# Performance work log

Measured on AMD Instinct MI355X. Metric: run time of the kernel, lower is better.

## Reference

```python
import jax, jax.numpy as jnp
import numpy as np

B, T, D = 4, 4096, 1024

def setup_inputs() -> dict:
    key = jax.random.key(0)
    ks = jax.random.split(key, 7)
    s1 = 1.0 / np.sqrt(D)
    s2 = 1.0 / np.sqrt(2 * D)
    return {
        "x": jax.random.normal(ks[0], (B, T, D), jnp.float32),
        "W1": jax.random.uniform(ks[1], (D, 2 * D), jnp.float32, -s1, s1),      # Linear(D,2D,bias=False)
        "W2": jax.random.uniform(ks[2], (2 * D, 2 * D), jnp.float32, -s2, s2),  # Linear(2D,2D)
        "b2": jax.random.uniform(ks[3], (2 * D,), jnp.float32, -s2, s2),
        "conv_w": jax.random.uniform(ks[4], (D, 1, 3), jnp.float32, -1/np.sqrt(3), 1/np.sqrt(3)),  # depthwise k=3
        "gamma": jnp.ones((D,), jnp.float32),
        "beta": jnp.zeros((D,), jnp.float32),
    }

def _gated_scan(theta, alpha):
    # parallel stable scan: h_t = a_t * h_{t-1} + (1 - a_t) * tanh(theta_t), h_0 = 0
    a = jax.nn.sigmoid(alpha)
    b = (1.0 - a) * jnp.tanh(theta)
    def combine(c1, c2):
        a1, b1 = c1
        a2, b2 = c2
        return a1 * a2, a2 * b1 + b2
    _, h = jax.lax.associative_scan(combine, (a, b), axis=1)
    return h

def reference(x, W1, W2, b2, conv_w, gamma, beta):
    # morphism generator: Linear -> SiLU -> Linear
    mp = jax.nn.silu(x @ W1) @ W2 + b2                      # (B,T,2D)
    theta, alpha = jnp.split(mp, 2, axis=-1)
    semantic = _gated_scan(theta, alpha)                    # (B,T,D)
    # causal depthwise conv: left-pad 2, kernel 3, groups=D
    sc = jnp.transpose(semantic, (0, 2, 1))                 # (B,D,T)
    cb = jax.lax.conv_general_dilated(
        sc, conv_w, window_strides=(1,), padding=[(2, 0)],
        dimension_numbers=("NCH", "OIH", "NCH"), feature_group_count=D)
    cb = jax.nn.silu(jnp.transpose(cb, (0, 2, 1)))          # (B,T,D)
    y = semantic + 0.1 * cb
    # LayerNorm over D
    mu = jnp.mean(y, axis=-1, keepdims=True)
    var = jnp.mean(jnp.square(y - mu), axis=-1, keepdims=True)
    y = (y - mu) * jax.lax.rsqrt(var + 1e-5) * gamma + beta
    # dropout is identity in eval mode; L2 normalize (torch eps=1e-12)
    nrm = jnp.sqrt(jnp.sum(jnp.square(y), axis=-1, keepdims=True))
    return y / jnp.maximum(nrm, 1e-12)
```

## Files before the change

kernel.cpp:

```cpp
#include <hip/hip_runtime.h>
#include <cstdint>
#include <cstddef>

typedef __attribute__((ext_vector_type(8))) short bf16x8;
typedef __attribute__((ext_vector_type(4))) float f32x4;
typedef unsigned short u16;
typedef unsigned int u32;

__device__ __forceinline__ u16 f2bf(float f) {
  u32 u = __float_as_uint(f);
  u32 r = (u + 0x7fffu + ((u >> 16) & 1u)) >> 16;
  return (u16)r;
}
__device__ __forceinline__ float bf2f(u16 h) {
  return __uint_as_float(((u32)h) << 16);
}
__device__ __forceinline__ float fsilu(float v) { return v / (1.f + __expf(-v)); }
__device__ __forceinline__ float fsigmoid(float v) { return 1.f / (1.f + __expf(-v)); }
__device__ __forceinline__ float ftanh(float v) {
  return 1.f - 2.f / (__expf(2.f * v) + 1.f);
}

__device__ __forceinline__ void glds16(const void* g, void* l) {
  __builtin_amdgcn_global_load_lds(
      (const __attribute__((address_space(1))) void*)g,
      (__attribute__((address_space(3))) void*)l, 16, 0, 0);
}

#define FENCE_MEM() asm volatile("" ::: "memory")
#define BAR() __builtin_amdgcn_s_barrier()
#define VMCNT(n) asm volatile("s_waitcnt vmcnt(" #n ")" ::: "memory")
#define LGKMW(n)                                        \
  do {                                                  \
    asm volatile("s_waitcnt lgkmcnt(" #n ")" ::: "memory"); \
    __builtin_amdgcn_sched_barrier(0);                  \
  } while (0)


__global__ __launch_bounds__(256) void cast_bf16_vec(const float* __restrict__ src,
                                                     u16* __restrict__ dst, int n4) {
  int i = blockIdx.x * 256 + threadIdx.x;
  if (i >= n4) return;
  const float4 v = ((const float4*)src)[i];
  ushort4 o;
  o.x = f2bf(v.x); o.y = f2bf(v.y); o.z = f2bf(v.z); o.w = f2bf(v.w);
  ((ushort4*)dst)[i] = o;
}

__global__ void transpose_cast(const float* __restrict__ src, u16* __restrict__ dst,
                               int R, int C) {
  __shared__ float tile[32][33];
  int bx = blockIdx.x * 32;
  int by = blockIdx.y * 32;
  int tx = threadIdx.x, ty = threadIdx.y;
#pragma unroll
  for (int i = 0; i < 4; ++i)
    tile[ty + i * 8][tx] = src[(size_t)(by + ty + i * 8) * C + bx + tx];
  __syncthreads();
#pragma unroll
  for (int i = 0; i < 4; ++i)
    dst[(size_t)(bx + ty + i * 8) * R + by + tx] = f2bf(tile[tx][ty + i * 8]);
}


template <int EPI>
__global__ __launch_bounds__(512, 2) void gemm256(const u16* __restrict__ A,
                                                  const u16* __restrict__ Bt,
                                                  u16* __restrict__ Co,
                                                  const float* __restrict__ bias,
                                                  int M, int N, int K) {
  __shared__ char lds[131072];
  const int tid = threadIdx.x;
  const int lane = tid & 63;
  const int wid = tid >> 6;
  const int wr = wid >> 2;
  const int wc = wid & 3;

  const int gx = gridDim.x;
  const int nwg = gx * gridDim.y;
  const int bid = blockIdx.y * gx + blockIdx.x;
  const int swz = (bid & 7) * (nwg >> 3) + (bid >> 3);
  const long bm = (long)(swz / gx) * 256;
  const long bn = (long)(swz % gx) * 256;

  const int NT = K >> 6;

  const int r0 = tid >> 3, c0p = tid & 7;
  const int r1 = r0 + 64;
  const int gA0 = (r0 & 63) + ((r0 >> 6) << 7);
  const int gA1 = (r1 & 63) + ((r1 >> 6) << 7);
  const int gB0 = (r0 & 31) + ((r0 >> 5) << 6);
  const int gB1 = (r1 & 31) + ((r1 >> 5) << 6);
  const int cA0 = c0p ^ (r0 & 7);
  const size_t srcA0 = (size_t)(bm + gA0) * K + cA0 * 8;
  const size_t srcA1 = (size_t)(bm + gA1) * K + cA0 * 8;
  const size_t srcB0 = (size_t)(bn + gB0) * K + cA0 * 8;
  const size_t srcB1 = (size_t)(bn + gB1) * K + cA0 * 8;
  const int dstA0 = gA0 * 128 + c0p * 16;
  const int dstA1 = gA1 * 128 + c0p * 16;
  const int dstB0 = 32768 + gB0 * 128 + c0p * 16;
  const int dstB1 = 32768 + gB1 * 128 + c0p * 16;
  const size_t halfA = (size_t)64 * K;
  const size_t halfB = (size_t)32 * K;

#define STAGE_P(buf, t, pair)                                                        \
  do {                                                                               \
    if ((pair) == 0) {                                                               \
      glds16(A + srcA0 + (size_t)(t) * 64, lds + (buf) * 65536 + dstA0);             \
      glds16(A + srcA1 + (size_t)(t) * 64, lds + (buf) * 65536 + dstA1);             \
    } else if ((pair) == 1) {                                                        \
      glds16(A + srcA0 + halfA + (size_t)(t) * 64,                                   \
             lds + (buf) * 65536 + dstA0 + 8192);                                    \
      glds16(A + srcA1 + halfA + (size_t)(t) * 64,                                   \
             lds + (buf) * 65536 + dstA1 + 8192);                                    \
    } else if ((pair) == 2) {                                                        \
      glds16(Bt + srcB0 + (size_t)(t) * 64, lds + (buf) * 65536 + dstB0);            \
      glds16(Bt + srcB1 + (size_t)(t) * 64, lds + (buf) * 65536 + dstB1);            \
    } else {                                                                         \
      glds16(Bt + srcB0 + halfB + (size_t)(t) * 64,                                  \
             lds + (buf) * 65536 + dstB0 + 4096);                                    \
      glds16(Bt + srcB1 + halfB + (size_t)(t) * 64,                                  \
             lds + (buf) * 65536 + dstB1 + 4096);                                    \
    }                                                                                \
  } while (0)

  const int l15 = lane & 15, l3 = lane & 7, g4 = lane >> 4;
  const int aoff0 = (wr * 128 + l15) * 128 + ((g4 ^ l3) * 16);
  const int aoff1 = (wr * 128 + l15) * 128 + (((4 + g4) ^ l3) * 16);
  const int boff0 = 32768 + (wc * 64 + l15) * 128 + ((g4 ^ l3) * 16);
  const int boff1 = 32768 + (wc * 64 + l15) * 128 + (((4 + g4) ^ l3) * 16);

  f32x4 acc[8][4] = {};

#define READ_A(dst, q)                                                               \
  do {                                                                               \
    dst[0][0] = *(const bf16x8*)(base + aoff0 + ((q) * 2 + 0) * 2048);               \
    dst[0][1] = *(const bf16x8*)(base + aoff1 + ((q) * 2 + 0) * 2048);               \
    dst[1][0] = *(const bf16x8*)(base + aoff0 + ((q) * 2 + 1) * 2048);               \
    dst[1][1] = *(const bf16x8*)(base + aoff1 + ((q) * 2 + 1) * 2048);               \
  } while (0)

#define MFMA_Q(q, af)                                                                \
  do {                                                                               \
    __builtin_amdgcn_s_setprio(1);                                                   \
    _Pragma("unroll") for (int kh = 0; kh < 2; ++kh)                                 \
        _Pragma("unroll") for (int mm = 0; mm < 2; ++mm)                             \
            _Pragma("unroll") for (int nn = 0; nn < 4; ++nn) {                       \
      acc[(q) * 2 + mm][nn] = __builtin_amdgcn_mfma_f32_16x16x32_bf16(               \
          af[mm][kh], bfr[nn][kh], acc[(q) * 2 + mm][nn], 0, 0, 0);                  \
    }                                                                                \
    __builtin_amdgcn_s_setprio(0);                                                   \
  } while (0)

  STAGE_P(0, 0, 0);
  STAGE_P(0, 0, 1);
  STAGE_P(0, 0, 2);
  STAGE_P(0, 0, 3);
  VMCNT(0);
  FENCE_MEM();
  BAR();
  FENCE_MEM();

  for (int t = 0; t < NT; ++t) {
    const int p = t & 1;
    const char* base = lds + p * 65536;
    const bool s1 = (t + 1) < NT;

    bf16x8 bfr[4][2];
    bf16x8 afx[2][2], afy[2][2];

#pragma unroll
    for (int nn = 0; nn < 4; ++nn) {
      bfr[nn][0] = *(const bf16x8*)(base + boff0 + nn * 2048);
      bfr[nn][1] = *(const bf16x8*)(base + boff1 + nn * 2048);
    }
    READ_A(afx, 0);
    READ_A(afy, 1);
    if (s1) STAGE_P(p ^ 1, t + 1, 0);
    FENCE_MEM();
    LGKMW(4);
    MFMA_Q(0, afx);
    READ_A(afx, 2);
    if (s1) STAGE_P(p ^ 1, t + 1, 1);
    FENCE_MEM();
    LGKMW(4);
    MFMA_Q(1, afy);
    READ_A(afy, 3);
    if (s1) STAGE_P(p ^ 1, t + 1, 2);
    FENCE_MEM();
    LGKMW(4);
    MFMA_Q(2, afx);
    if (s1) STAGE_P(p ^ 1, t + 1, 3);
    FENCE_MEM();
    LGKMW(0);
    MFMA_Q(3, afy);

    VMCNT(0);
    FENCE_MEM();
    BAR();
    FENCE_MEM();
  }

  const int erow = (lane >> 4) * 4;
  const int ecol = lane & 15;
#pragma unroll
  for (int mf = 0; mf < 8; ++mf) {
#pragma unroll
    for (int nf = 0; nf < 4; ++nf) {
      const long col = bn + wc * 64 + nf * 16 + ecol;
      float badd = (EPI == 1) ? bias[col] : 0.f;
#pragma unroll
      for (int j = 0; j < 4; ++j) {
        const long row = bm + wr * 128 + mf * 16 + erow + j;
        float v = acc[mf][nf][j];
        if (EPI == 0) {
          v = fsilu(v);
        } else {
          v += badd;
          v = (col < 1024) ? ftanh(v) : fsigmoid(v);
        }
        Co[row * (long)N + col] = f2bf(v);
      }
    }
  }
#undef STAGE_P
#undef READ_A
#undef MFMA_Q
}


__global__ __launch_bounds__(256) void scan_stage1(const u16* __restrict__ sa,
                                                   float* __restrict__ cA,
                                                   float* __restrict__ cB,
                                                   float* __restrict__ cA63,
                                                   float* __restrict__ cB63) {
  const int tid = blockIdx.x * 256 + threadIdx.x;
  const int d = tid & 1023;
  const int chunk = (tid >> 10) & 63;
  const int b = tid >> 16;
  const size_t base = ((size_t)(b * 4096 + chunk * 64)) * 2048 + d;
  float Ac = 1.f, Bc = 0.f;
#pragma unroll 4
  for (int t = 0; t < 63; ++t) {
    float s = bf2f(sa[base + (size_t)t * 2048]);
    float a = bf2f(sa[base + (size_t)t * 2048 + 1024]);
    Bc = a * Bc + (1.f - a) * s;
    Ac *= a;
  }
  cA63[tid] = Ac;
  cB63[tid] = Bc;
  {
    float s = bf2f(sa[base + (size_t)63 * 2048]);
    float a = bf2f(sa[base + (size_t)63 * 2048 + 1024]);
    Bc = a * Bc + (1.f - a) * s;
    Ac *= a;
  }
  cA[tid] = Ac;
  cB[tid] = Bc;
}

__global__ __launch_bounds__(256) void scan_stage2(const float* __restrict__ cA,
                                                   const float* __restrict__ cB,
                                                   float* __restrict__ hstart) {
  const int tid = blockIdx.x * 256 + threadIdx.x;
  const int d = tid & 1023;
  const int b = tid >> 10;
  float h = 0.f;
  for (int c = 0; c < 64; ++c) {
    const size_t i = ((size_t)(b * 64 + c)) * 1024 + d;
    hstart[i] = h;
    h = cA[i] * h + cB[i];
  }
}

__global__ __launch_bounds__(256) void scan3_fused(
    const u16* __restrict__ sa, const float* __restrict__ hstart,
    const float* __restrict__ cA63, const float* __restrict__ cB63,
    const float* __restrict__ cw, const float* __restrict__ gamma,
    const float* __restrict__ beta, float* __restrict__ out) {
  const int blk = blockIdx.x;
  const int c = blk & 63;
  const int tid = threadIdx.x;
  const int lane = tid & 63, wid = tid >> 6;
  const int d0 = tid * 4;
  const size_t m0 = (size_t)(blk >> 6) * 4096 + (size_t)c * 64;

  __shared__ float red[4][8];

  const float4 gv = *(const float4*)(gamma + d0);
  const float4 bv = *(const float4*)(beta + d0);
  const float g[4] = {gv.x, gv.y, gv.z, gv.w};
  const float be[4] = {bv.x, bv.y, bv.z, bv.w};
  float w0[4], w1[4], w2[4];
#pragma unroll
  for (int j = 0; j < 4; ++j) {
    w0[j] = cw[(d0 + j) * 3];
    w1[j] = cw[(d0 + j) * 3 + 1];
    w2[j] = cw[(d0 + j) * 3 + 2];
  }

  const size_t hidx = (size_t)blk * 1024 + d0;
  const float4 hs = *(const float4*)(hstart + hidx);
  float h1v[4] = {hs.x, hs.y, hs.z, hs.w};
  float h2v[4] = {0.f, 0.f, 0.f, 0.f};
  if (c > 0) {
    const float4 hp = *(const float4*)(hstart + hidx - 1024);
    const float4 a63 = *(const float4*)(cA63 + hidx - 1024);
    const float4 b63 = *(const float4*)(cB63 + hidx - 1024);
    h2v[0] = a63.x * hp.x + b63.x;
    h2v[1] = a63.y * hp.y + b63.y;
    h2v[2] = a63.z * hp.z + b63.z;
    h2v[3] = a63.w * hp.w + b63.w;
  }

  float sg2 = 0.f, sgb = 0.f, sb2 = 0.f;
#pragma unroll
  for (int j = 0; j < 4; ++j) {
    sg2 += g[j] * g[j];
    sgb += g[j] * be[j];
    sb2 += be[j] * be[j];
  }
#pragma unroll
  for (int o = 32; o > 0; o >>= 1) {
    sg2 += __shfl_down(sg2, o);
    sgb += __shfl_down(sgb, o);
    sb2 += __shfl_down(sb2, o);
  }
  if (lane == 0) { red[wid][5] = sg2; red[wid][6] = sgb; red[wid][7] = sb2; }
  __syncthreads();
  const float Sg2 = red[0][5] + red[1][5] + red[2][5] + red[3][5];
  const float Sgb = red[0][6] + red[1][6] + red[2][6] + red[3][6];
  const float Sb2 = red[0][7] + red[1][7] + red[2][7] + red[3][7];
  __syncthreads();

  const u16* ps = sa + m0 * 2048 + d0;
  ushort4 sv = *(const ushort4*)(ps);
  ushort4 av = *(const ushort4*)(ps + 1024);

  for (int t = 0; t < 64; ++t) {
    ushort4 svn, avn;
    if (t + 1 < 64) {
      svn = *(const ushort4*)(ps + (size_t)(t + 1) * 2048);
      avn = *(const ushort4*)(ps + (size_t)(t + 1) * 2048 + 1024);
    }
    const float sarr[4] = {bf2f(sv.x), bf2f(sv.y), bf2f(sv.z), bf2f(sv.w)};
    const float aarr[4] = {bf2f(av.x), bf2f(av.y), bf2f(av.z), bf2f(av.w)};
    float y[4];
    float s1 = 0.f, s2 = 0.f, g1 = 0.f, g2 = 0.f, gb = 0.f;
#pragma unroll
    for (int j = 0; j < 4; ++j) {
      const float a = aarr[j];
      const float h = a * h1v[j] + (1.f - a) * sarr[j];
      float cb = w0[j] * h2v[j] + w1[j] * h1v[j] + w2[j] * h;
      cb = fsilu(cb);
      y[j] = h + 0.1f * cb;
      h2v[j] = h1v[j];
      h1v[j] = h;
      s1 += y[j];
      s2 += y[j] * y[j];
      const float gy = g[j] * y[j];
      g1 += g[j] * gy;
      g2 += gy * gy;
      gb += be[j] * gy;
    }
    float v0 = s1, v1 = s2, v2 = g1, v3 = g2, v4 = gb;
#pragma unroll
    for (int o = 32; o > 0; o >>= 1) {
      v0 += __shfl_down(v0, o);
      v1 += __shfl_down(v1, o);
      v2 += __shfl_down(v2, o);
      v3 += __shfl_down(v3, o);
      v4 += __shfl_down(v4, o);
    }
    if (lane == 0) {
      red[wid][0] = v0; red[wid][1] = v1; red[wid][2] = v2;
      red[wid][3] = v3; red[wid][4] = v4;
    }
    __syncthreads();
    const float S1 = red[0][0] + red[1][0] + red[2][0] + red[3][0];
    const float S2 = red[0][1] + red[1][1] + red[2][1] + red[3][1];
    const float G1 = red[0][2] + red[1][2] + red[2][2] + red[3][2];
    const float G2 = red[0][3] + red[1][3] + red[2][3] + red[3][3];
    const float GB = red[0][4] + red[1][4] + red[2][4] + red[3][4];
    const float mu = S1 * (1.f / 1024.f);
    const float var = S2 * (1.f / 1024.f) - mu * mu;
    const float rstd = rsqrtf(var + 1e-5f);
    const float sge2 = G2 - 2.f * mu * G1 + mu * mu * Sg2;
    const float sgbe = GB - mu * Sgb;
    const float nrm2 = rstd * rstd * sge2 + 2.f * rstd * sgbe + Sb2;
    const float nrm = sqrtf(fmaxf(nrm2, 0.f));
    const float scale = 1.f / fmaxf(nrm, 1e-12f);
    float4 o4;
    o4.x = (g[0] * (y[0] - mu) * rstd + be[0]) * scale;
    o4.y = (g[1] * (y[1] - mu) * rstd + be[1]) * scale;
    o4.z = (g[2] * (y[2] - mu) * rstd + be[2]) * scale;
    o4.w = (g[3] * (y[3] - mu) * rstd + be[3]) * scale;
    *(float4*)(out + (m0 + t) * 1024 + d0) = o4;
    __syncthreads();
    sv = svn;
    av = avn;
  }
}


extern "C" void kernel_launch(void* const* d_in, const int* in_sizes, int n_in,
                              void* d_out, int out_size, void* d_ws, size_t ws_size,
                              hipStream_t stream) {
  const float* x = (const float*)d_in[0];
  const float* W1 = (const float*)d_in[1];
  const float* W2 = (const float*)d_in[2];
  const float* b2 = (const float*)d_in[3];
  const float* cw = (const float*)d_in[4];
  const float* gamma = (const float*)d_in[5];
  const float* beta = (const float*)d_in[6];
  float* out = (float*)d_out;
  char* ws = (char*)d_ws;

  u16* xb = (u16*)(ws);
  u16* w1t = (u16*)(ws + 33554432);
  u16* w2t = (u16*)(ws + 37748736);
  u16* h1 = (u16*)(ws + 46137344);
  u16* sa = (u16*)(ws + 113246208);
  float* cA = (float*)(ws);
  float* cB = (float*)(ws + 1048576);
  float* hstart = (float*)(ws + 2097152);
  float* cA63 = (float*)(ws + 3145728);
  float* cB63 = (float*)(ws + 4194304);

  cast_bf16_vec<<<16384, 256, 0, stream>>>(x, xb, 4194304);
  transpose_cast<<<dim3(64, 32), dim3(32, 8), 0, stream>>>(W1, w1t, 1024, 2048);
  transpose_cast<<<dim3(64, 64), dim3(32, 8), 0, stream>>>(W2, w2t, 2048, 2048);
  gemm256<0><<<dim3(8, 64), 512, 0, stream>>>(xb, w1t, h1, nullptr, 16384, 2048, 1024);
  gemm256<1><<<dim3(8, 64), 512, 0, stream>>>(h1, w2t, sa, b2, 16384, 2048, 2048);
  scan_stage1<<<1024, 256, 0, stream>>>(sa, cA, cB, cA63, cB63);
  scan_stage2<<<16, 256, 0, stream>>>(cA, cB, hstart);
  scan3_fused<<<256, 256, 0, stream>>>(sa, hstart, cA63, cB63, cw, gamma, beta, out);
}
```

Measured before the change: 329.5 us.

## Use 32x32x16 MFMA in GEMM, vectorize scan stage1, fold stage2 into scan3

The GEMM inner loop moves from 16x16x32 to 32x32x16 bf16 MFMA tiles, which changes fragment loads and the epilogue row mapping. The aim is fewer LDS reads and fewer MFMA issues per output. Scan stage1 now processes four channels per thread with vector loads and launches fewer blocks. The serial stage2 kernel is removed and each scan3 block recomputes its chunk prefix from the chunk aggregates, trading a kernel launch for redundant per-block work.

After: 369.6 us. 12.2% more time.

```diff
diff --git a/kernel.cpp b/kernel.cpp
--- a/kernel.cpp
+++ b/kernel.cpp
@@ -3,7 +3,7 @@
 #include <cstddef>
 
 typedef __attribute__((ext_vector_type(8))) short bf16x8;
-typedef __attribute__((ext_vector_type(4))) float f32x4;
+typedef __attribute__((ext_vector_type(16))) float f32x16;
 typedef unsigned short u16;
 typedef unsigned int u32;
 
@@ -124,30 +124,31 @@
     }                                                                                \
   } while (0)
 
-  const int l15 = lane & 15, l3 = lane & 7, g4 = lane >> 4;
-  const int aoff0 = (wr * 128 + l15) * 128 + ((g4 ^ l3) * 16);
-  const int aoff1 = (wr * 128 + l15) * 128 + (((4 + g4) ^ l3) * 16);
-  const int boff0 = 32768 + (wc * 64 + l15) * 128 + ((g4 ^ l3) * 16);
-  const int boff1 = 32768 + (wc * 64 + l15) * 128 + (((4 + g4) ^ l3) * 16);
-
-  f32x4 acc[8][4] = {};
-
-#define READ_A(dst, q)                                                               \
+  const int l31 = lane & 31, l7 = lane & 7, kg = lane >> 5;
+  const int abase = (wr * 128 + l31) * 128;
+  const int bbase = 32768 + (wc * 64 + l31) * 128;
+  const int cof0 = ((0 + kg) ^ l7) * 16;
+  const int cof1 = ((2 + kg) ^ l7) * 16;
+  const int cof2 = ((4 + kg) ^ l7) * 16;
+  const int cof3 = ((6 + kg) ^ l7) * 16;
+
+  f32x16 acc[4][2] = {};
+
+#define COF(ks) ((ks) == 0 ? cof0 : (ks) == 1 ? cof1 : (ks) == 2 ? cof2 : cof3)
+
+#define READ_A(dst, ks)                                                              \
   do {                                                                               \
-    dst[0][0] = *(const bf16x8*)(base + aoff0 + ((q) * 2 + 0) * 2048);               \
-    dst[0][1] = *(const bf16x8*)(base + aoff1 + ((q) * 2 + 0) * 2048);               \
-    dst[1][0] = *(const bf16x8*)(base + aoff0 + ((q) * 2 + 1) * 2048);               \
-    dst[1][1] = *(const bf16x8*)(base + aoff1 + ((q) * 2 + 1) * 2048);               \
+    _Pragma("unroll") for (int mf = 0; mf < 4; ++mf)                                 \
+        dst[mf] = *(const bf16x8*)(base + abase + mf * 32 * 128 + COF(ks));          \
   } while (0)
 
-#define MFMA_Q(q, af)                                                                \
+#define MFMA_G(ks, af)                                                               \
   do {                                                                               \
     __builtin_amdgcn_s_setprio(1);                                                   \
-    _Pragma("unroll") for (int kh = 0; kh < 2; ++kh)                                 \
-        _Pragma("unroll") for (int mm = 0; mm < 2; ++mm)                             \
-            _Pragma("unroll") for (int nn = 0; nn < 4; ++nn) {                       \
-      acc[(q) * 2 + mm][nn] = __builtin_amdgcn_mfma_f32_16x16x32_bf16(               \
-          af[mm][kh], bfr[nn][kh], acc[(q) * 2 + mm][nn], 0, 0, 0);                  \
+    _Pragma("unroll") for (int mf = 0; mf < 4; ++mf)                                 \
+        _Pragma("unroll") for (int nf = 0; nf < 2; ++nf) {                           \
+      acc[mf][nf] = __builtin_amdgcn_mfma_f32_32x32x16_bf16(                         \
+          af[mf], bfr[nf][ks], acc[mf][nf], 0, 0, 0);                                \
     }                                                                                \
     __builtin_amdgcn_s_setprio(0);                                                   \
   } while (0)
@@ -166,34 +167,36 @@
     const char* base = lds + p * 65536;
     const bool s1 = (t + 1) < NT;
 
-    bf16x8 bfr[4][2];
-    bf16x8 afx[2][2], afy[2][2];
-
-#pragma unroll
-    for (int nn = 0; nn < 4; ++nn) {
-      bfr[nn][0] = *(const bf16x8*)(base + boff0 + nn * 2048);
-      bfr[nn][1] = *(const bf16x8*)(base + boff1 + nn * 2048);
-    }
-    READ_A(afx, 0);
-    READ_A(afy, 1);
+    bf16x8 bfr[2][4];
+    bf16x8 ax[4], ay[4];
+
+#pragma unroll
+    for (int nf = 0; nf < 2; ++nf) {
+      bfr[nf][0] = *(const bf16x8*)(base + bbase + nf * 32 * 128 + cof0);
+      bfr[nf][1] = *(const bf16x8*)(base + bbase + nf * 32 * 128 + cof1);
+      bfr[nf][2] = *(const bf16x8*)(base + bbase + nf * 32 * 128 + cof2);
+      bfr[nf][3] = *(const bf16x8*)(base + bbase + nf * 32 * 128 + cof3);
+    }
+    READ_A(ax, 0);
+    READ_A(ay, 1);
     if (s1) STAGE_P(p ^ 1, t + 1, 0);
     FENCE_MEM();
     LGKMW(4);
-    MFMA_Q(0, afx);
-    READ_A(afx, 2);
+    MFMA_G(0, ax);
+    READ_A(ax, 2);
     if (s1) STAGE_P(p ^ 1, t + 1, 1);
     FENCE_MEM();
     LGKMW(4);
-    MFMA_Q(1, afy);
-    READ_A(afy, 3);
+    MFMA_G(1, ay);
+    READ_A(ay, 3);
     if (s1) STAGE_P(p ^ 1, t + 1, 2);
     FENCE_MEM();
     LGKMW(4);
-    MFMA_Q(2, afx);
+    MFMA_G(2, ax);
     if (s1) STAGE_P(p ^ 1, t + 1, 3);
     FENCE_MEM();
     LGKMW(0);
-    MFMA_Q(3, afy);
+    MFMA_G(3, ay);
 
     VMCNT(0);
     FENCE_MEM();
@@ -201,18 +204,17 @@
     FENCE_MEM();
   }
 
-  const int erow = (lane >> 4) * 4;
-  const int ecol = lane & 15;
-#pragma unroll
-  for (int mf = 0; mf < 8; ++mf) {
-#pragma unroll
-    for (int nf = 0; nf < 4; ++nf) {
-      const long col = bn + wc * 64 + nf * 16 + ecol;
+#pragma unroll
+  for (int mf = 0; mf < 4; ++mf) {
+#pragma unroll
+    for (int nf = 0; nf < 2; ++nf) {
+      const long col = bn + wc * 64 + nf * 32 + l31;
       float badd = (EPI == 1) ? bias[col] : 0.f;
 #pragma unroll
-      for (int j = 0; j < 4; ++j) {
-        const long row = bm + wr * 128 + mf * 16 + erow + j;
-        float v = acc[mf][nf][j];
+      for (int reg = 0; reg < 16; ++reg) {
+        const long row =
+            bm + wr * 128 + mf * 32 + (reg & 3) + 8 * (reg >> 2) + 4 * kg;
+        float v = acc[mf][nf][reg];
         if (EPI == 0) {
           v = fsilu(v);
         } else {
@@ -225,7 +227,8 @@
   }
 #undef STAGE_P
 #undef READ_A
-#undef MFMA_Q
+#undef MFMA_G
+#undef COF
 }
 
 
@@ -235,49 +238,49 @@
                                                    float* __restrict__ cA63,
                                                    float* __restrict__ cB63) {
   const int tid = blockIdx.x * 256 + threadIdx.x;
-  const int d = tid & 1023;
-  const int chunk = (tid >> 10) & 63;
-  const int b = tid >> 16;
-  const size_t base = ((size_t)(b * 4096 + chunk * 64)) * 2048 + d;
-  float Ac = 1.f, Bc = 0.f;
+  const int d0 = (tid & 255) * 4;
+  const int chunk = (tid >> 8) & 63;
+  const int b = tid >> 14;
+  const size_t row0 = (size_t)(b * 4096 + chunk * 64);
+  const u16* ps = sa + row0 * 2048 + d0;
+  float Ac[4] = {1.f, 1.f, 1.f, 1.f};
+  float Bc[4] = {0.f, 0.f, 0.f, 0.f};
 #pragma unroll 4
   for (int t = 0; t < 63; ++t) {
-    float s = bf2f(sa[base + (size_t)t * 2048]);
-    float a = bf2f(sa[base + (size_t)t * 2048 + 1024]);
-    Bc = a * Bc + (1.f - a) * s;
-    Ac *= a;
-  }
-  cA63[tid] = Ac;
-  cB63[tid] = Bc;
+    const ushort4 sv = *(const ushort4*)(ps + (size_t)t * 2048);
+    const ushort4 av = *(const ushort4*)(ps + (size_t)t * 2048 + 1024);
+    const float s[4] = {bf2f(sv.x), bf2f(sv.y), bf2f(sv.z), bf2f(sv.w)};
+    const float a[4] = {bf2f(av.x), bf2f(av.y), bf2f(av.z), bf2f(av.w)};
+#pragma unroll
+    for (int j = 0; j < 4; ++j) {
+      Bc[j] = a[j] * Bc[j] + (1.f - a[j]) * s[j];
+      Ac[j] *= a[j];
+    }
+  }
+  const size_t cidx = (size_t)(b * 64 + chunk) * 1024 + d0;
+  *(float4*)(cA63 + cidx) = make_float4(Ac[0], Ac[1], Ac[2], Ac[3]);
+  *(float4*)(cB63 + cidx) = make_float4(Bc[0], Bc[1], Bc[2], Bc[3]);
   {
-    float s = bf2f(sa[base + (size_t)63 * 2048]);
-    float a = bf2f(sa[base + (size_t)63 * 2048 + 1024]);
-    Bc = a * Bc + (1.f - a) * s;
-    Ac *= a;
-  }
-  cA[tid] = Ac;
-  cB[tid] = Bc;
-}
-
-__global__ __launch_bounds__(256) void scan_stage2(const float* __restrict__ cA,
-                                                   const float* __restrict__ cB,
-                                                   float* __restrict__ hstart) {
-  const int tid = blockIdx.x * 256 + threadIdx.x;
-  const int d = tid & 1023;
-  const int b = tid >> 10;
-  float h = 0.f;
-  for (int c = 0; c < 64; ++c) {
-    const size_t i = ((size_t)(b * 64 + c)) * 1024 + d;
-    hstart[i] = h;
-    h = cA[i] * h + cB[i];
-  }
+    const ushort4 sv = *(const ushort4*)(ps + (size_t)63 * 2048);
+    const ushort4 av = *(const ushort4*)(ps + (size_t)63 * 2048 + 1024);
+    const float s[4] = {bf2f(sv.x), bf2f(sv.y), bf2f(sv.z), bf2f(sv.w)};
+    const float a[4] = {bf2f(av.x), bf2f(av.y), bf2f(av.z), bf2f(av.w)};
+#pragma unroll
+    for (int j = 0; j < 4; ++j) {
+      Bc[j] = a[j] * Bc[j] + (1.f - a[j]) * s[j];
+      Ac[j] *= a[j];
+    }
+  }
+  *(float4*)(cA + cidx) = make_float4(Ac[0], Ac[1], Ac[2], Ac[3]);
+  *(float4*)(cB + cidx) = make_float4(Bc[0], Bc[1], Bc[2], Bc[3]);
 }
 
 __global__ __launch_bounds__(256) void scan3_fused(
-    const u16* __restrict__ sa, const float* __restrict__ hstart,
-    const float* __restrict__ cA63, const float* __restrict__ cB63,
-    const float* __restrict__ cw, const float* __restrict__ gamma,
-    const float* __restrict__ beta, float* __restrict__ out) {
+    const u16* __restrict__ sa, const float* __restrict__ cA,
+    const float* __restrict__ cB, const float* __restrict__ cA63,
+    const float* __restrict__ cB63, const float* __restrict__ cw,
+    const float* __restrict__ gamma, const float* __restrict__ beta,
+    float* __restrict__ out) {
   const int blk = blockIdx.x;
   const int c = blk & 63;
   const int tid = threadIdx.x;
@@ -299,18 +302,30 @@
     w2[j] = cw[(d0 + j) * 3 + 2];
   }
 
-  const size_t hidx = (size_t)blk * 1024 + d0;
-  const float4 hs = *(const float4*)(hstart + hidx);
-  float h1v[4] = {hs.x, hs.y, hs.z, hs.w};
+  float hcur[4] = {0.f, 0.f, 0.f, 0.f};
+  float hp[4] = {0.f, 0.f, 0.f, 0.f};
+  const size_t chbase = (size_t)(blk - c) * 1024 + d0;
+  for (int i = 0; i < c; ++i) {
+    const float4 a4 = *(const float4*)(cA + chbase + (size_t)i * 1024);
+    const float4 b4 = *(const float4*)(cB + chbase + (size_t)i * 1024);
+    if (i == c - 1) {
+      hp[0] = hcur[0]; hp[1] = hcur[1]; hp[2] = hcur[2]; hp[3] = hcur[3];
+    }
+    hcur[0] = a4.x * hcur[0] + b4.x;
+    hcur[1] = a4.y * hcur[1] + b4.y;
+    hcur[2] = a4.z * hcur[2] + b4.z;
+    hcur[3] = a4.w * hcur[3] + b4.w;
+  }
+  float h1v[4] = {hcur[0], hcur[1], hcur[2], hcur[3]};
   float h2v[4] = {0.f, 0.f, 0.f, 0.f};
   if (c > 0) {
-    const float4 hp = *(const float4*)(hstart + hidx - 1024);
-    const float4 a63 = *(const float4*)(cA63 + hidx - 1024);
-    const float4 b63 = *(const float4*)(cB63 + hidx - 1024);
-    h2v[0] = a63.x * hp.x + b63.x;
-    h2v[1] = a63.y * hp.y + b63.y;
-    h2v[2] = a63.z * hp.z + b63.z;
-    h2v[3] = a63.w * hp.w + b63.w;
+    const size_t pidx = (size_t)(blk - 1) * 1024 + d0;
+    const float4 a63 = *(const float4*)(cA63 + pidx);
+    const float4 b63 = *(const float4*)(cB63 + pidx);
+    h2v[0] = a63.x * hp[0] + b63.x;
+    h2v[1] = a63.y * hp[1] + b63.y;
+    h2v[2] = a63.z * hp[2] + b63.z;
+    h2v[3] = a63.w * hp[3] + b63.w;
   }
 
   float sg2 = 0.f, sgb = 0.f, sb2 = 0.f;
@@ -423,16 +438,14 @@
   u16* sa = (u16*)(ws + 113246208);
   float* cA = (float*)(ws);
   float* cB = (float*)(ws + 1048576);
-  float* hstart = (float*)(ws + 2097152);
-  float* cA63 = (float*)(ws + 3145728);
-  float* cB63 = (float*)(ws + 4194304);
+  float* cA63 = (float*)(ws + 2097152);
+  float* cB63 = (float*)(ws + 3145728);
 
   cast_bf16_vec<<<16384, 256, 0, stream>>>(x, xb, 4194304);
   transpose_cast<<<dim3(64, 32), dim3(32, 8), 0, stream>>>(W1, w1t, 1024, 2048);
   transpose_cast<<<dim3(64, 64), dim3(32, 8), 0, stream>>>(W2, w2t, 2048, 2048);
   gemm256<0><<<dim3(8, 64), 512, 0, stream>>>(xb, w1t, h1, nullptr, 16384, 2048, 1024);
   gemm256<1><<<dim3(8, 64), 512, 0, stream>>>(h1, w2t, sa, b2, 16384, 2048, 2048);
-  scan_stage1<<<1024, 256, 0, stream>>>(sa, cA, cB, cA63, cB63);
-  scan_stage2<<<16, 256, 0, stream>>>(cA, cB, hstart);
-  scan3_fused<<<256, 256, 0, stream>>>(sa, hstart, cA63, cB63, cw, gamma, beta, out);
-}
+  scan_stage1<<<256, 256, 0, stream>>>(sa, cA, cB, cA63, cB63);
+  scan3_fused<<<256, 256, 0, stream>>>(sa, cA, cB, cA63, cB63, cw, gamma, beta, out);
+}
```
